# Performance work log

Hardware: AMD Instinct MI355X
Metric: run time of the kernel (lower is better)

Reference implementation:

```python
import jax, jax.numpy as jnp
import numpy as np

EPS = 1e-10


def setup_inputs() -> dict:
    key = jax.random.key(0)
    ks = jax.random.split(key, 8)
    b, s, m, r, n = 2, 2048, 1024, 64, 16
    u = jax.random.normal(ks[0], (b, s, m), dtype=jnp.float32)
    delta = jax.random.normal(ks[1], (b, s, r), dtype=jnp.float32)
    dt_proj_w = jax.random.normal(ks[2], (m, r), dtype=jnp.float32) * 0.02
    dt_proj_b = jax.random.normal(ks[3], (m,), dtype=jnp.float32) * 0.02
    # A_log ~ Uniform(-3, -1) as in nn.init.uniform_(self.A_log, -3.0, -1.0)
    A_log = jax.random.uniform(ks[4], (n, m), dtype=jnp.float32, minval=-3.0, maxval=-1.0)
    D_skip = jnp.ones((m,), dtype=jnp.float32)
    # xavier_uniform with gain=0.1 on [n, m]
    bound = 0.1 * np.sqrt(6.0 / (n + m))
    B_proj_w = jax.random.uniform(ks[5], (n, m), dtype=jnp.float32, minval=-bound, maxval=bound)
    C_proj_w = jax.random.uniform(ks[6], (n, m), dtype=jnp.float32, minval=-bound, maxval=bound)
    return {"u": u, "delta": delta, "dt_proj_w": dt_proj_w, "dt_proj_b": dt_proj_b,
            "A_log": A_log, "D_skip": D_skip, "B_proj_w": B_proj_w, "C_proj_w": C_proj_w}


def reference(u, delta, dt_proj_w, dt_proj_b, A_log, D_skip, B_proj_w, C_proj_w):
    # u: [b, s, m]; delta: [b, s, r]
    dt = jax.nn.softplus(jnp.einsum('bsr,mr->bsm', delta, dt_proj_w) + dt_proj_b)
    dt = jnp.clip(dt, 1e-6, 10.0)                      # [b, s, m]
    A = jnp.clip(-jnp.exp(A_log), -10.0, -1e-6)        # [n, m]
    B = jnp.einsum('bsm,nm->bsn', u, B_proj_w)         # [b, s, n]
    C = jnp.einsum('bsm,nm->bsn', u, C_proj_w)         # [b, s, n]

    # associative-scan path (seq_len > 256), math as in _associative_scan:
    # h_t = exp(cumsum_t log(dA)) * cumsum_t (dB_u / dA)
    dA = jnp.exp(dt[:, :, None, :] * A[None, None])    # [b, s, n, m]
    dA_c = jnp.clip(dA, EPS, None)
    dBu = dt[:, :, None, :] * B[..., None] * u[:, :, None, :]  # [b, s, n, m]
    A_cum = jnp.exp(jnp.cumsum(jnp.log(dA_c), axis=1))
    h = A_cum * jnp.cumsum(dBu / dA_c, axis=1)          # [b, s, n, m]
    y = jnp.einsum('bsnm,bsn->bsm', h, C)               # contract state dim

    out = y + u * D_skip
    out = jnp.clip(out, -10000.0, 10000.0)
    bad = jnp.any(~jnp.isfinite(out))
    return jnp.where(bad, jnp.zeros_like(u), out)
```

## Files before the change

### kernel.cpp

```cpp
#include <hip/hip_runtime.h>
#include <hip/hip_bf16.h>
#include <math.h>

#define B_ 2
#define S_ 2048
#define M_ 1024
#define R_ 64
#define N_ 16
#define NC 64
#define CH (S_/NC)

#define DT_OFF  0
#define BP_OFF  4194304
#define CP_OFF  4259840
#define BWT_OFF 4325376
#define CWT_OFF 4341760
#define P_OFF   4358144

__global__ __launch_bounds__(256) void k_transpose(const float* __restrict__ Bw,
                                                   const float* __restrict__ Cw,
                                                   float* __restrict__ BwT,
                                                   float* __restrict__ CwT) {
    int idx = blockIdx.x * 256 + threadIdx.x;
    if (idx >= M_ * N_) return;
    int m = idx >> 4, n = idx & 15;
    BwT[idx] = Bw[n * M_ + m];
    CwT[idx] = Cw[n * M_ + m];
}

__global__ __launch_bounds__(256) void k_dt(const float* __restrict__ delta,
                                            const float* __restrict__ Wdt,
                                            const float* __restrict__ bdt,
                                            float* __restrict__ dt) {
    int m    = blockIdx.x * 256 + threadIdx.x;
    int row0 = blockIdx.y * 32;
    float w[R_];
    const float4* W4 = reinterpret_cast<const float4*>(Wdt + m * R_);
#pragma unroll
    for (int i = 0; i < R_ / 4; ++i) {
        float4 v = W4[i];
        w[4*i] = v.x; w[4*i+1] = v.y; w[4*i+2] = v.z; w[4*i+3] = v.w;
    }
    float bias = bdt[m];
    for (int r = 0; r < 32; ++r) {
        int bs = row0 + r;
        const float* dr = delta + bs * R_;
        float acc = bias;
#pragma unroll
        for (int k = 0; k < R_; ++k) acc = fmaf(dr[k], w[k], acc);
        float sp = fmaxf(acc, 0.f) + log1pf(expf(-fabsf(acc)));
        sp = fminf(fmaxf(sp, 1e-6f), 10.0f);
        dt[bs * M_ + m] = sp;
    }
}

__global__ __launch_bounds__(256) void k_bc(const float* __restrict__ u,
                                            const float* __restrict__ BwT,
                                            const float* __restrict__ CwT,
                                            float* __restrict__ Bp,
                                            float* __restrict__ Cp) {
    __shared__ float uLds[16 * 1024];
    int base = blockIdx.x * 16;
    for (int i = threadIdx.x; i < 16 * 1024; i += 256)
        uLds[i] = u[base * M_ + i];
    __syncthreads();
    int r = threadIdx.x >> 4, n = threadIdx.x & 15;
    const float4* u4 = reinterpret_cast<const float4*>(uLds + r * 1024);
    float accB = 0.f, accC = 0.f;
#pragma unroll 4
    for (int m4 = 0; m4 < 256; ++m4) {
        float4 uv = u4[m4];
        int mb = m4 * 4;
        accB = fmaf(uv.x, BwT[(mb+0)*16 + n], accB);
        accB = fmaf(uv.y, BwT[(mb+1)*16 + n], accB);
        accB = fmaf(uv.z, BwT[(mb+2)*16 + n], accB);
        accB = fmaf(uv.w, BwT[(mb+3)*16 + n], accB);
        accC = fmaf(uv.x, CwT[(mb+0)*16 + n], accC);
        accC = fmaf(uv.y, CwT[(mb+1)*16 + n], accC);
        accC = fmaf(uv.z, CwT[(mb+2)*16 + n], accC);
        accC = fmaf(uv.w, CwT[(mb+3)*16 + n], accC);
    }
    Bp[(base + r) * N_ + n] = accB;
    Cp[(base + r) * N_ + n] = accC;
}

__device__ __forceinline__ void load_row16(const float* __restrict__ p, float* dst) {
    const float4* p4 = reinterpret_cast<const float4*>(p);
#pragma unroll
    for (int i = 0; i < 4; ++i) {
        float4 v = p4[i];
        dst[4*i] = v.x; dst[4*i+1] = v.y; dst[4*i+2] = v.z; dst[4*i+3] = v.w;
    }
}

__global__ __launch_bounds__(256) void k_pass1(const float* __restrict__ dt,
                                               const float* __restrict__ u,
                                               const float* __restrict__ Bp,
                                               const float* __restrict__ A_log,
                                               float* __restrict__ P) {
    int m = blockIdx.x * 256 + threadIdx.x;
    int c = blockIdx.y, b = blockIdx.z;
    float Aa[N_];
#pragma unroll
    for (int n = 0; n < N_; ++n) {
        float a = -expf(A_log[n * M_ + m]);
        Aa[n] = fminf(fmaxf(a, -10.f), -1e-6f);
    }
    float sL[N_], sS[N_];
#pragma unroll
    for (int n = 0; n < N_; ++n) { sL[n] = 0.f; sS[n] = 0.f; }
    int s0 = c * CH;
    for (int i = 0; i < CH; ++i) {
        int s = s0 + i;
        int off = (b * S_ + s) * M_ + m;
        float dtv = dt[off], uv = u[off];
        float du = dtv * uv;
        float bv[N_];
        load_row16(Bp + (b * S_ + s) * N_, bv);
#pragma unroll
        for (int n = 0; n < N_; ++n) {
            float a = dtv * Aa[n];
            sL[n] += a;
            sS[n] = fmaf(du * bv[n], __expf(-a), sS[n]);
        }
    }
#pragma unroll
    for (int n = 0; n < N_; ++n) {
        P[((b * 32 + n)      * NC + c) * M_ + m] = sL[n];
        P[((b * 32 + 16 + n) * NC + c) * M_ + m] = sS[n];
    }
}

__global__ __launch_bounds__(256) void k_scanchunks(float* __restrict__ P) {
    int x = blockIdx.x * 256 + threadIdx.x;
    int m = x & (M_ - 1);
    int j = (x >> 10) & 31;
    int b = x >> 15;
    int base = ((b * 32 + j) * NC) * M_ + m;
    float run = 0.f;
    for (int c = 0; c < NC; ++c) {
        float v = P[base + c * M_];
        P[base + c * M_] = run;
        run += v;
    }
}

__global__ __launch_bounds__(256) void k_pass3(const float* __restrict__ dt,
                                               const float* __restrict__ u,
                                               const float* __restrict__ Bp,
                                               const float* __restrict__ Cp,
                                               const float* __restrict__ A_log,
                                               const float* __restrict__ Dskip,
                                               const float* __restrict__ P,
                                               float* __restrict__ out) {
    int m = blockIdx.x * 256 + threadIdx.x;
    int c = blockIdx.y, b = blockIdx.z;
    float Aa[N_];
#pragma unroll
    for (int n = 0; n < N_; ++n) {
        float a = -expf(A_log[n * M_ + m]);
        Aa[n] = fminf(fmaxf(a, -10.f), -1e-6f);
    }
    float L[N_], Sv[N_];
#pragma unroll
    for (int n = 0; n < N_; ++n) {
        L[n]  = P[((b * 32 + n)      * NC + c) * M_ + m];
        Sv[n] = P[((b * 32 + 16 + n) * NC + c) * M_ + m];
    }
    float Dm = Dskip[m];
    int s0 = c * CH;
    for (int i = 0; i < CH; ++i) {
        int s = s0 + i;
        int off = (b * S_ + s) * M_ + m;
        float dtv = dt[off], uv = u[off];
        float du = dtv * uv;
        float bv[N_], cv[N_];
        load_row16(Bp + (b * S_ + s) * N_, bv);
        load_row16(Cp + (b * S_ + s) * N_, cv);
        float y = 0.f;
#pragma unroll
        for (int n = 0; n < N_; ++n) {
            float a = dtv * Aa[n];
            L[n] += a;
            Sv[n] = fmaf(du * bv[n], __expf(-a), Sv[n]);
            y = fmaf(__expf(L[n]) * Sv[n], cv[n], y);
        }
        float o = y + uv * Dm;
        o = fminf(fmaxf(o, -10000.f), 10000.f);
        out[off] = o;
    }
}

extern "C" void kernel_launch(void* const* d_in, const int* in_sizes, int n_in,
                              void* d_out, int out_size, void* d_ws, size_t ws_size,
                              hipStream_t stream) {
    const float* u     = (const float*)d_in[0];
    const float* delta = (const float*)d_in[1];
    const float* Wdt   = (const float*)d_in[2];
    const float* bdt   = (const float*)d_in[3];
    const float* A_log = (const float*)d_in[4];
    const float* Dski  = (const float*)d_in[5];
    const float* Bw    = (const float*)d_in[6];
    const float* Cw    = (const float*)d_in[7];
    float* out = (float*)d_out;
    float* ws  = (float*)d_ws;

    float* dt  = ws + DT_OFF;
    float* Bp  = ws + BP_OFF;
    float* Cp  = ws + CP_OFF;
    float* BwT = ws + BWT_OFF;
    float* CwT = ws + CWT_OFF;
    float* P   = ws + P_OFF;

    k_transpose<<<64, 256, 0, stream>>>(Bw, Cw, BwT, CwT);
    k_dt<<<dim3(4, 128), 256, 0, stream>>>(delta, Wdt, bdt, dt);
    k_bc<<<256, 256, 0, stream>>>(u, BwT, CwT, Bp, Cp);
    k_pass1<<<dim3(4, NC, B_), 256, 0, stream>>>(dt, u, Bp, A_log, P);
    k_scanchunks<<<256, 256, 0, stream>>>(P);
    k_pass3<<<dim3(4, NC, B_), 256, 0, stream>>>(dt, u, Bp, Cp, A_log, Dski, P, out);
}
```

Before: 127.4 us.

## Restructure scan pipeline: split-K B/C projection, n-split threads, multiplicative chunk carries

Splits the B/C projection over four K slices with a separate reduce kernel, and cuts rows per block in the dt kernel so more blocks launch. Rewrites the chunked scan so each thread handles four state channels of one column, staging dt/u/B/C in LDS and combining the four channel groups with cross-lane shuffles. Carries are now a (decay product, state) pair scanned multiplicatively instead of log-sum plus scaled sum, which removes the exp(-a) and exp(L) per element. This raises parallelism and lowers per-thread register pressure, at the cost of extra kernels, extra workspace traffic and different numerics.

Result: faster. 114.7 us (-9.9%).

```diff
diff --git a/kernel.cpp b/kernel.cpp
--- a/kernel.cpp
+++ b/kernel.cpp
@@ -11,18 +11,20 @@
 #define CH (S_/NC)
 
 #define DT_OFF  0
-#define BP_OFF  4194304
-#define CP_OFF  4259840
-#define BWT_OFF 4325376
-#define CWT_OFF 4341760
-#define P_OFF   4358144
-
-__global__ __launch_bounds__(256) void k_transpose(const float* __restrict__ Bw,
-                                                   const float* __restrict__ Cw,
-                                                   float* __restrict__ BwT,
-                                                   float* __restrict__ CwT) {
+#define P_OFF   4194304
+#define H_OFF   6291456
+#define BP_OFF  8388608
+#define CP_OFF  8454144
+#define BWT_OFF 8519680
+#define CWT_OFF 8536064
+#define PB_OFF  8552448
+#define PC_OFF  8814592
+
+__global__ __launch_bounds__(256) void k_prep(const float* __restrict__ Bw,
+                                              const float* __restrict__ Cw,
+                                              float* __restrict__ BwT,
+                                              float* __restrict__ CwT) {
     int idx = blockIdx.x * 256 + threadIdx.x;
-    if (idx >= M_ * N_) return;
     int m = idx >> 4, n = idx & 15;
     BwT[idx] = Bw[n * M_ + m];
     CwT[idx] = Cw[n * M_ + m];
@@ -33,115 +35,150 @@
                                             const float* __restrict__ bdt,
                                             float* __restrict__ dt) {
     int m    = blockIdx.x * 256 + threadIdx.x;
-    int row0 = blockIdx.y * 32;
+    int row0 = blockIdx.y * 8;
     float w[R_];
-    const float4* W4 = reinterpret_cast<const float4*>(Wdt + m * R_);
+    const float4* W4 = reinterpret_cast<const float4*>(Wdt + (size_t)m * R_);
 #pragma unroll
     for (int i = 0; i < R_ / 4; ++i) {
         float4 v = W4[i];
         w[4*i] = v.x; w[4*i+1] = v.y; w[4*i+2] = v.z; w[4*i+3] = v.w;
     }
     float bias = bdt[m];
-    for (int r = 0; r < 32; ++r) {
+#pragma unroll 1
+    for (int r = 0; r < 8; ++r) {
         int bs = row0 + r;
-        const float* dr = delta + bs * R_;
+        const float* dr = delta + (size_t)bs * R_;
         float acc = bias;
 #pragma unroll
         for (int k = 0; k < R_; ++k) acc = fmaf(dr[k], w[k], acc);
         float sp = fmaxf(acc, 0.f) + log1pf(expf(-fabsf(acc)));
         sp = fminf(fmaxf(sp, 1e-6f), 10.0f);
-        dt[bs * M_ + m] = sp;
-    }
-}
-
-__global__ __launch_bounds__(256) void k_bc(const float* __restrict__ u,
-                                            const float* __restrict__ BwT,
-                                            const float* __restrict__ CwT,
-                                            float* __restrict__ Bp,
-                                            float* __restrict__ Cp) {
-    __shared__ float uLds[16 * 1024];
-    int base = blockIdx.x * 16;
-    for (int i = threadIdx.x; i < 16 * 1024; i += 256)
-        uLds[i] = u[base * M_ + i];
+        dt[(size_t)bs * M_ + m] = sp;
+    }
+}
+
+__global__ __launch_bounds__(256) void k_bc_partial(const float* __restrict__ u,
+                                                    const float* __restrict__ BwT,
+                                                    const float* __restrict__ CwT,
+                                                    float* __restrict__ pB,
+                                                    float* __restrict__ pC) {
+    __shared__ float uLds[16 * 260];
+    int r0 = blockIdx.x * 16;
+    int k0 = blockIdx.y * 256;
+    for (int i = threadIdx.x; i < 4096; i += 256) {
+        int r = i >> 8, k = i & 255;
+        uLds[r * 260 + k] = u[(size_t)(r0 + r) * M_ + k0 + k];
+    }
     __syncthreads();
     int r = threadIdx.x >> 4, n = threadIdx.x & 15;
-    const float4* u4 = reinterpret_cast<const float4*>(uLds + r * 1024);
+    const float4* u4 = reinterpret_cast<const float4*>(uLds + r * 260);
     float accB = 0.f, accC = 0.f;
 #pragma unroll 4
-    for (int m4 = 0; m4 < 256; ++m4) {
-        float4 uv = u4[m4];
-        int mb = m4 * 4;
-        accB = fmaf(uv.x, BwT[(mb+0)*16 + n], accB);
-        accB = fmaf(uv.y, BwT[(mb+1)*16 + n], accB);
-        accB = fmaf(uv.z, BwT[(mb+2)*16 + n], accB);
-        accB = fmaf(uv.w, BwT[(mb+3)*16 + n], accB);
-        accC = fmaf(uv.x, CwT[(mb+0)*16 + n], accC);
-        accC = fmaf(uv.y, CwT[(mb+1)*16 + n], accC);
-        accC = fmaf(uv.z, CwT[(mb+2)*16 + n], accC);
-        accC = fmaf(uv.w, CwT[(mb+3)*16 + n], accC);
-    }
-    Bp[(base + r) * N_ + n] = accB;
-    Cp[(base + r) * N_ + n] = accC;
-}
-
-__device__ __forceinline__ void load_row16(const float* __restrict__ p, float* dst) {
-    const float4* p4 = reinterpret_cast<const float4*>(p);
-#pragma unroll
-    for (int i = 0; i < 4; ++i) {
-        float4 v = p4[i];
-        dst[4*i] = v.x; dst[4*i+1] = v.y; dst[4*i+2] = v.z; dst[4*i+3] = v.w;
-    }
+    for (int k4 = 0; k4 < 64; ++k4) {
+        float4 uv = u4[k4];
+        int kb = k0 + k4 * 4;
+        accB = fmaf(uv.x, BwT[(kb+0)*16 + n], accB);
+        accB = fmaf(uv.y, BwT[(kb+1)*16 + n], accB);
+        accB = fmaf(uv.z, BwT[(kb+2)*16 + n], accB);
+        accB = fmaf(uv.w, BwT[(kb+3)*16 + n], accB);
+        accC = fmaf(uv.x, CwT[(kb+0)*16 + n], accC);
+        accC = fmaf(uv.y, CwT[(kb+1)*16 + n], accC);
+        accC = fmaf(uv.z, CwT[(kb+2)*16 + n], accC);
+        accC = fmaf(uv.w, CwT[(kb+3)*16 + n], accC);
+    }
+    size_t o = (size_t)blockIdx.y * 65536 + (size_t)(r0 + r) * 16 + n;
+    pB[o] = accB;
+    pC[o] = accC;
+}
+
+__global__ __launch_bounds__(256) void k_bc_reduce(const float* __restrict__ pB,
+                                                   const float* __restrict__ pC,
+                                                   float* __restrict__ Bp,
+                                                   float* __restrict__ Cp) {
+    int idx = blockIdx.x * 256 + threadIdx.x;
+    float sB = 0.f, sC = 0.f;
+#pragma unroll
+    for (int ks = 0; ks < 4; ++ks) {
+        sB += pB[(size_t)ks * 65536 + idx];
+        sC += pC[(size_t)ks * 65536 + idx];
+    }
+    Bp[idx] = sB;
+    Cp[idx] = sC;
 }
 
 __global__ __launch_bounds__(256) void k_pass1(const float* __restrict__ dt,
                                                const float* __restrict__ u,
                                                const float* __restrict__ Bp,
                                                const float* __restrict__ A_log,
-                                               float* __restrict__ P) {
-    int m = blockIdx.x * 256 + threadIdx.x;
-    int c = blockIdx.y, b = blockIdx.z;
-    float Aa[N_];
-#pragma unroll
-    for (int n = 0; n < N_; ++n) {
-        float a = -expf(A_log[n * M_ + m]);
-        Aa[n] = fminf(fmaxf(a, -10.f), -1e-6f);
-    }
-    float sL[N_], sS[N_];
-#pragma unroll
-    for (int n = 0; n < N_; ++n) { sL[n] = 0.f; sS[n] = 0.f; }
+                                               float* __restrict__ P,
+                                               float* __restrict__ H) {
+    __shared__ float ldsDt[CH * 64], ldsU[CH * 64], ldsB[CH * 16];
+    int m0 = blockIdx.x * 64, c = blockIdx.y, b = blockIdx.z;
     int s0 = c * CH;
-    for (int i = 0; i < CH; ++i) {
-        int s = s0 + i;
-        int off = (b * S_ + s) * M_ + m;
-        float dtv = dt[off], uv = u[off];
-        float du = dtv * uv;
-        float bv[N_];
-        load_row16(Bp + (b * S_ + s) * N_, bv);
-#pragma unroll
-        for (int n = 0; n < N_; ++n) {
-            float a = dtv * Aa[n];
-            sL[n] += a;
-            sS[n] = fmaf(du * bv[n], __expf(-a), sS[n]);
-        }
-    }
-#pragma unroll
-    for (int n = 0; n < N_; ++n) {
-        P[((b * 32 + n)      * NC + c) * M_ + m] = sL[n];
-        P[((b * 32 + 16 + n) * NC + c) * M_ + m] = sS[n];
-    }
-}
-
-__global__ __launch_bounds__(256) void k_scanchunks(float* __restrict__ P) {
-    int x = blockIdx.x * 256 + threadIdx.x;
-    int m = x & (M_ - 1);
-    int j = (x >> 10) & 31;
-    int b = x >> 15;
-    int base = ((b * 32 + j) * NC) * M_ + m;
-    float run = 0.f;
-    for (int c = 0; c < NC; ++c) {
-        float v = P[base + c * M_];
-        P[base + c * M_] = run;
-        run += v;
+    int tid = threadIdx.x;
+    for (int i = tid; i < CH * 64; i += 256) {
+        int s = i >> 6, ml = i & 63;
+        size_t off = ((size_t)(b * S_ + s0 + s)) * M_ + m0 + ml;
+        ldsDt[i] = dt[off];
+        ldsU[i]  = u[off];
+    }
+    for (int i = tid; i < CH * 16; i += 256)
+        ldsB[i] = Bp[(size_t)(b * S_ + s0) * N_ + i];
+    __syncthreads();
+    int lane = tid & 63, wave = tid >> 6;
+    int ml = wave * 16 + (lane & 15);
+    int m  = m0 + ml;
+    int n0 = (lane >> 4) * 4;
+    float Aa[4], h[4] = {0,0,0,0}, g[4] = {1.f,1.f,1.f,1.f};
+#pragma unroll
+    for (int j = 0; j < 4; ++j) {
+        float a = -expf(A_log[(size_t)(n0 + j) * M_ + m]);
+        Aa[j] = fminf(fmaxf(a, -10.f), -1e-6f);
+    }
+    for (int s = 0; s < CH; ++s) {
+        float dtv = ldsDt[s * 64 + ml];
+        float uv  = ldsU [s * 64 + ml];
+        float du  = dtv * uv;
+        float4 bv = *reinterpret_cast<const float4*>(&ldsB[s * 16 + n0]);
+        float bb[4] = {bv.x, bv.y, bv.z, bv.w};
+#pragma unroll
+        for (int j = 0; j < 4; ++j) {
+            float ea = __expf(dtv * Aa[j]);
+            h[j] = fmaf(ea, h[j], g[j] * (du * bb[j]));
+            g[j] *= ea;
+        }
+    }
+#pragma unroll
+    for (int j = 0; j < 4; ++j) {
+        size_t o = ((size_t)(b * 16 + n0 + j) * NC + c) * M_ + m;
+        P[o] = g[j];
+        H[o] = h[j];
+    }
+}
+
+__global__ __launch_bounds__(256) void k_pass2(float* __restrict__ P,
+                                               float* __restrict__ H) {
+    int idx = blockIdx.x * 256 + threadIdx.x;
+    int m = idx & (M_ - 1);
+    int n = (idx >> 10) & 15;
+    int b = idx >> 14;
+    size_t base = ((size_t)(b * 16 + n) * NC) * M_ + m;
+    float grun = 1.f, hrun = 0.f;
+#pragma unroll 1
+    for (int c0 = 0; c0 < NC; c0 += 8) {
+        float pv[8], hv[8];
+#pragma unroll
+        for (int t = 0; t < 8; ++t) {
+            pv[t] = P[base + (size_t)(c0 + t) * M_];
+            hv[t] = H[base + (size_t)(c0 + t) * M_];
+        }
+#pragma unroll
+        for (int t = 0; t < 8; ++t) {
+            P[base + (size_t)(c0 + t) * M_] = grun;
+            H[base + (size_t)(c0 + t) * M_] = hrun;
+            hrun = fmaf(pv[t], hrun, grun * hv[t]);
+            grun *= pv[t];
+        }
     }
 }
 
@@ -151,43 +188,61 @@
                                                const float* __restrict__ Cp,
                                                const float* __restrict__ A_log,
                                                const float* __restrict__ Dskip,
-                                               const float* __restrict__ P,
+                                               const float* __restrict__ Pinit,
+                                               const float* __restrict__ Hinit,
                                                float* __restrict__ out) {
-    int m = blockIdx.x * 256 + threadIdx.x;
-    int c = blockIdx.y, b = blockIdx.z;
-    float Aa[N_];
-#pragma unroll
-    for (int n = 0; n < N_; ++n) {
-        float a = -expf(A_log[n * M_ + m]);
-        Aa[n] = fminf(fmaxf(a, -10.f), -1e-6f);
-    }
-    float L[N_], Sv[N_];
-#pragma unroll
-    for (int n = 0; n < N_; ++n) {
-        L[n]  = P[((b * 32 + n)      * NC + c) * M_ + m];
-        Sv[n] = P[((b * 32 + 16 + n) * NC + c) * M_ + m];
+    __shared__ float ldsDt[CH * 64], ldsU[CH * 64], ldsB[CH * 16], ldsC[CH * 16];
+    int m0 = blockIdx.x * 64, c = blockIdx.y, b = blockIdx.z;
+    int s0 = c * CH;
+    int tid = threadIdx.x;
+    for (int i = tid; i < CH * 64; i += 256) {
+        int s = i >> 6, ml = i & 63;
+        size_t off = ((size_t)(b * S_ + s0 + s)) * M_ + m0 + ml;
+        ldsDt[i] = dt[off];
+        ldsU[i]  = u[off];
+    }
+    for (int i = tid; i < CH * 16; i += 256) {
+        ldsB[i] = Bp[(size_t)(b * S_ + s0) * N_ + i];
+        ldsC[i] = Cp[(size_t)(b * S_ + s0) * N_ + i];
+    }
+    __syncthreads();
+    int lane = tid & 63, wave = tid >> 6;
+    int ml = wave * 16 + (lane & 15);
+    int m  = m0 + ml;
+    int ng = lane >> 4, n0 = ng * 4;
+    float Aa[4], h[4], g[4];
+#pragma unroll
+    for (int j = 0; j < 4; ++j) {
+        float a = -expf(A_log[(size_t)(n0 + j) * M_ + m]);
+        Aa[j] = fminf(fmaxf(a, -10.f), -1e-6f);
+        size_t o = ((size_t)(b * 16 + n0 + j) * NC + c) * M_ + m;
+        g[j] = Pinit[o];
+        h[j] = Hinit[o];
     }
     float Dm = Dskip[m];
-    int s0 = c * CH;
-    for (int i = 0; i < CH; ++i) {
-        int s = s0 + i;
-        int off = (b * S_ + s) * M_ + m;
-        float dtv = dt[off], uv = u[off];
-        float du = dtv * uv;
-        float bv[N_], cv[N_];
-        load_row16(Bp + (b * S_ + s) * N_, bv);
-        load_row16(Cp + (b * S_ + s) * N_, cv);
+    for (int s = 0; s < CH; ++s) {
+        float dtv = ldsDt[s * 64 + ml];
+        float uv  = ldsU [s * 64 + ml];
+        float du  = dtv * uv;
+        float4 bv = *reinterpret_cast<const float4*>(&ldsB[s * 16 + n0]);
+        float4 cv = *reinterpret_cast<const float4*>(&ldsC[s * 16 + n0]);
+        float bb[4] = {bv.x, bv.y, bv.z, bv.w};
+        float cc[4] = {cv.x, cv.y, cv.z, cv.w};
         float y = 0.f;
 #pragma unroll
-        for (int n = 0; n < N_; ++n) {
-            float a = dtv * Aa[n];
-            L[n] += a;
-            Sv[n] = fmaf(du * bv[n], __expf(-a), Sv[n]);
-            y = fmaf(__expf(L[n]) * Sv[n], cv[n], y);
-        }
-        float o = y + uv * Dm;
-        o = fminf(fmaxf(o, -10000.f), 10000.f);
-        out[off] = o;
+        for (int j = 0; j < 4; ++j) {
+            float ea = __expf(dtv * Aa[j]);
+            h[j] = fmaf(ea, h[j], g[j] * (du * bb[j]));
+            g[j] *= ea;
+            y = fmaf(h[j], cc[j], y);
+        }
+        y += __shfl_xor(y, 16, 64);
+        y += __shfl_xor(y, 32, 64);
+        if (ng == 0) {
+            float o = y + uv * Dm;
+            o = fminf(fmaxf(o, -10000.f), 10000.f);
+            out[((size_t)(b * S_ + s0 + s)) * M_ + m] = o;
+        }
     }
 }
 
@@ -206,16 +261,20 @@
     float* ws  = (float*)d_ws;
 
     float* dt  = ws + DT_OFF;
+    float* P   = ws + P_OFF;
+    float* H   = ws + H_OFF;
     float* Bp  = ws + BP_OFF;
     float* Cp  = ws + CP_OFF;
     float* BwT = ws + BWT_OFF;
     float* CwT = ws + CWT_OFF;
-    float* P   = ws + P_OFF;
-
-    k_transpose<<<64, 256, 0, stream>>>(Bw, Cw, BwT, CwT);
-    k_dt<<<dim3(4, 128), 256, 0, stream>>>(delta, Wdt, bdt, dt);
-    k_bc<<<256, 256, 0, stream>>>(u, BwT, CwT, Bp, Cp);
-    k_pass1<<<dim3(4, NC, B_), 256, 0, stream>>>(dt, u, Bp, A_log, P);
-    k_scanchunks<<<256, 256, 0, stream>>>(P);
-    k_pass3<<<dim3(4, NC, B_), 256, 0, stream>>>(dt, u, Bp, Cp, A_log, Dski, P, out);
-}
+    float* pB  = ws + PB_OFF;
+    float* pC  = ws + PC_OFF;
+
+    k_prep<<<64, 256, 0, stream>>>(Bw, Cw, BwT, CwT);
+    k_dt<<<dim3(4, 512), 256, 0, stream>>>(delta, Wdt, bdt, dt);
+    k_bc_partial<<<dim3(256, 4), 256, 0, stream>>>(u, BwT, CwT, pB, pC);
+    k_bc_reduce<<<256, 256, 0, stream>>>(pB, pC, Bp, Cp);
+    k_pass1<<<dim3(16, NC, B_), 256, 0, stream>>>(dt, u, Bp, A_log, P, H);
+    k_pass2<<<128, 256, 0, stream>>>(P, H);
+    k_pass3<<<dim3(16, NC, B_), 256, 0, stream>>>(dt, u, Bp, Cp, A_log, Dski, P, H, out);
+}
```
